# Optimization experiments

Hardware: AMD Instinct MI355X
Metric: run time of the kernel (lower is better)

The kernel has to match this reference:

```python
import jax, jax.numpy as jnp
import numpy as np

D_DIM, H_DIM, W_DIM = 8, 16, 16
HIDDEN, HEAD = 256, 32
NUM_HEADS = HIDDEN // HEAD


def _rel_indices(D, H, W):
    # 3D relative coordinate indices into the bias table, shape (N, N) each.
    coords = np.stack(np.meshgrid(np.arange(D), np.arange(H), np.arange(W), indexing='ij'),
                      axis=-1).reshape(-1, 3)
    rel = coords[:, None, :] - coords[None, :, :]
    rel[:, :, 0] += D - 1
    rel[:, :, 1] += H - 1
    rel[:, :, 2] += W - 1
    return jnp.asarray(rel[:, :, 0]), jnp.asarray(rel[:, :, 1]), jnp.asarray(rel[:, :, 2])


def setup_inputs() -> dict:
    key = jax.random.key(0)
    ks = jax.random.split(key, 6)
    B = 4
    x = jax.random.normal(ks[0], (B, D_DIM, H_DIM, W_DIM, HIDDEN), dtype=jnp.float32)
    s = 1.0 / np.sqrt(HIDDEN)
    Wq = jax.random.normal(ks[1], (HIDDEN, HIDDEN), dtype=jnp.float32) * s
    Wk = jax.random.normal(ks[2], (HIDDEN, HIDDEN), dtype=jnp.float32) * s
    Wv = jax.random.normal(ks[3], (HIDDEN, HIDDEN), dtype=jnp.float32) * s
    Wo = jax.random.normal(ks[4], (HIDDEN, HIDDEN), dtype=jnp.float32) * s
    bias_table = jax.random.normal(ks[5], (NUM_HEADS, 2 * D_DIM - 1, 2 * H_DIM - 1, 2 * W_DIM - 1),
                                   dtype=jnp.float32) * 0.02
    return {"x": x, "Wq": Wq, "Wk": Wk, "Wv": Wv, "Wo": Wo, "bias_table": bias_table}


def reference(x, Wq, Wk, Wv, Wo, bias_table):
    B, D, H, W, C = x.shape
    N = D * H * W
    rd, rh, rw = _rel_indices(D, H, W)
    # gathered relative-position bias: (num_heads, N, N)
    bias = bias_table[:, rd, rh, rw]

    xf = x.reshape(B, N, C)
    q = (xf @ Wq).reshape(B, N, NUM_HEADS, HEAD).transpose(0, 2, 1, 3)  # b h n d
    k = (xf @ Wk).reshape(B, N, NUM_HEADS, HEAD).transpose(0, 2, 1, 3)
    v = (xf @ Wv).reshape(B, N, NUM_HEADS, HEAD).transpose(0, 2, 1, 3)

    scores = jnp.einsum('bhnd,bhmd->bhnm', q, k) / jnp.sqrt(jnp.float32(HEAD))
    scores = scores + bias[None]  # broadcast over batch
    attn = jax.nn.softmax(scores, axis=-1)
    out = jnp.einsum('bhnm,bhmd->bhnd', attn, v)
    out = out.transpose(0, 2, 1, 3).reshape(B, N, HIDDEN) @ Wo
    return out.reshape(B, D, H, W, HIDDEN)
```

## Files before the change

kernel.cpp:

```cpp
#include <hip/hip_runtime.h>
#include <math.h>

#define HIDDEN 256
#define NHEADS 8
#define HEAD 32
#define NTOK 2048
#define NBIAS 115320
#define HTAB 14415

typedef __attribute__((ext_vector_type(8))) __bf16 bf16x8;
typedef __attribute__((ext_vector_type(4))) float f32x4;
typedef __attribute__((ext_vector_type(16))) float f32x16;
typedef __attribute__((ext_vector_type(4))) unsigned uint32x4;

static __device__ __forceinline__ f32x4 mfma16(bf16x8 a, bf16x8 b, f32x4 c) {
    return __builtin_amdgcn_mfma_f32_16x16x32_bf16(a, b, c, 0, 0, 0);
}
static __device__ __forceinline__ f32x16 mfma32(bf16x8 a, bf16x8 b, f32x16 c) {
    return __builtin_amdgcn_mfma_f32_32x32x16_bf16(a, b, c, 0, 0, 0);
}
static __device__ __forceinline__ float fexp2(float x) {
#if __has_builtin(__builtin_amdgcn_exp2f)
    return __builtin_amdgcn_exp2f(x);
#else
    return exp2f(x);
#endif
}
static __device__ __forceinline__ unsigned pkbf16(float a, float b) {
    unsigned short ua = __builtin_bit_cast(unsigned short, (__bf16)a);
    unsigned short ub = __builtin_bit_cast(unsigned short, (__bf16)b);
    return (unsigned)ua | ((unsigned)ub << 16);
}

__global__ void k_cvt_x(const float* __restrict__ x, __bf16* __restrict__ xb) {
    int i = (blockIdx.x * blockDim.x + threadIdx.x) * 4;
    float4 v = *(const float4*)(x + i);
    xb[i + 0] = (__bf16)v.x;
    xb[i + 1] = (__bf16)v.y;
    xb[i + 2] = (__bf16)v.z;
    xb[i + 3] = (__bf16)v.w;
}

__global__ void k_cvt_w(const float* __restrict__ w0, const float* __restrict__ w1,
                        const float* __restrict__ w2, const float* __restrict__ w3,
                        __bf16* __restrict__ t0, __bf16* __restrict__ t1,
                        __bf16* __restrict__ t2, __bf16* __restrict__ t3) {
    int wsel = blockIdx.x >> 8;
    int i = (blockIdx.x & 255) * 256 + threadIdx.x;
    const float* w = (wsel == 0) ? w0 : (wsel == 1) ? w1 : (wsel == 2) ? w2 : w3;
    __bf16* t = (wsel == 0) ? t0 : (wsel == 1) ? t1 : (wsel == 2) ? t2 : t3;
    int n = i >> 8, k = i & 255;
    t[i] = (__bf16)w[k * 256 + n];
}

__global__ __launch_bounds__(256) void k_qkv(const __bf16* __restrict__ xb,
                                             const __bf16* __restrict__ wqT,
                                             const __bf16* __restrict__ wkT,
                                             const __bf16* __restrict__ wvT,
                                             __bf16* __restrict__ qb,
                                             __bf16* __restrict__ kb,
                                             __bf16* __restrict__ vb) {
    int wid = blockIdx.x * 4 + (threadIdx.x >> 6);
    int lane = threadIdx.x & 63;
    int ng = wid % 12, mt = wid / 12;
    int lm = lane & 15, lg = lane >> 4, lk = lg * 8;
    int which = ng >> 2;
    int nc0 = (ng & 3) * 64;
    const __bf16* wT = (which == 0) ? wqT : (which == 1) ? wkT : wvT;

    f32x4 acc[4][4];
#pragma unroll
    for (int m = 0; m < 4; ++m)
#pragma unroll
        for (int n = 0; n < 4; ++n) acc[m][n] = (f32x4){0.f, 0.f, 0.f, 0.f};

    const __bf16* arow = xb + (size_t)(mt * 64 + lm) * 256 + lk;
    const __bf16* brow = wT + (size_t)(nc0 + lm) * 256 + lk;
#pragma unroll
    for (int kk = 0; kk < 8; ++kk) {
        bf16x8 a[4], b[4];
#pragma unroll
        for (int m = 0; m < 4; ++m) a[m] = *(const bf16x8*)(arow + (size_t)m * 16 * 256 + kk * 32);
#pragma unroll
        for (int n = 0; n < 4; ++n) b[n] = *(const bf16x8*)(brow + (size_t)n * 16 * 256 + kk * 32);
#pragma unroll
        for (int m = 0; m < 4; ++m)
#pragma unroll
            for (int n = 0; n < 4; ++n) acc[m][n] = mfma16(a[m], b[n], acc[m][n]);
    }
    const float QS = 0.17677669529663687f * 1.4426950408889634f;
#pragma unroll
    for (int m = 0; m < 4; ++m) {
#pragma unroll
        for (int n = 0; n < 4; ++n) {
            int col = nc0 + n * 16 + lm;
            int h = col >> 5, d = col & 31;
#pragma unroll
            for (int r = 0; r < 4; ++r) {
                int row = mt * 64 + m * 16 + lg * 4 + r;
                int b_ = row >> 11, tr = row & 2047;
                size_t bh = (size_t)(b_ * 8 + h) * 65536;
                if (which == 0) {
                    qb[bh + (size_t)tr * 32 + d] = (__bf16)(acc[m][n][r] * QS);
                } else if (which == 1) {
                    size_t idx = ((size_t)(tr >> 5) * 128 + (d >> 4) * 64 + ((d >> 3) & 1) * 32 + (tr & 31)) * 8 + (d & 7);
                    kb[bh + idx] = (__bf16)acc[m][n][r];
                } else {
                    size_t idx = ((size_t)(tr >> 5) * 256 + ((tr >> 3) & 3) * 64 + ((tr >> 2) & 1) * 32 + d) * 4 + (tr & 3);
                    vb[bh + idx] = (__bf16)acc[m][n][r];
                }
            }
        }
    }
}

__global__ __launch_bounds__(256) void k_attn(const __bf16* __restrict__ qb,
                                              const __bf16* __restrict__ kb,
                                              const __bf16* __restrict__ vb,
                                              const float* __restrict__ bias,
                                              __bf16* __restrict__ attn) {
    int i = blockIdx.x;
    int bh = (i & 7) + ((i >> 9) << 3);
    int qs = (i >> 3) & 63;
    int b_ = bh >> 3, h = bh & 7;
    int w = threadIdx.x >> 6;
    int lane = threadIdx.x & 63;
    int lq = lane & 31;
    int hf = lane >> 5;
    int q0 = qs * 32;

    __shared__ float smem[4488];

    {
        int qd = q0 >> 8, qh0 = (q0 >> 4) & 15;
        const float* bt = bias + h * HTAB;
        for (int t = threadIdx.x; t < 4488; t += 256) {
            int dd = t / 561, rem = t - dd * 561;
            int hh = rem / 33, ww = rem - hh * 33;
            int dw = 30 - ww; if (dw < 0) dw = 0;
            smem[t] = bt[(qd + dd) * 961 + (qh0 + hh) * 31 + dw] * 1.4426950408889634f;
        }
    }
    __syncthreads();

    const __bf16* qbase = qb + (size_t)bh * NTOK * 32;
    const __bf16* kbase = kb + (size_t)bh * NTOK * 32;
    const __bf16* vbase = vb + (size_t)bh * NTOK * 32;

    bf16x8 qf0 = *(const bf16x8*)(qbase + (size_t)(q0 + lq) * 32 + hf * 8);
    bf16x8 qf1 = *(const bf16x8*)(qbase + (size_t)(q0 + lq) * 32 + 16 + hf * 8);

    int lbase = (lq >> 4) * 33 + 15 - (lq & 15) + 4 * hf;

    f32x16 Oacc, Lacc;
#pragma unroll
    for (int j = 0; j < 16; ++j) { Oacc[j] = 0.f; Lacc[j] = 0.f; }

    bf16x8 ones;
#pragma unroll
    for (int j = 0; j < 8; ++j) ones[j] = (__bf16)1.0f;

    bf16x8 ck0, ck1;
    {
        const __bf16* kt = kbase + ((size_t)(w * 16) * 128 + lane) * 8;
        ck0 = *(const bf16x8*)(kt);
        ck1 = *(const bf16x8*)(kt + 512);
    }

#pragma unroll
    for (int it = 0; it < 16; ++it) {
        int t0 = w * 512 + it * 32;
        int tt = t0 >> 5;

        bf16x8 nk0, nk1;
        if (it < 15) {
            const __bf16* kt1 = kbase + ((size_t)(tt + 1) * 128 + lane) * 8;
            nk0 = *(const bf16x8*)(kt1);
            nk1 = *(const bf16x8*)(kt1 + 512);
        }

        const __bf16* vt = vbase + ((size_t)tt * 256 + lane) * 4;
        uint2 va  = *(const uint2*)(vt);
        uint2 vbq = *(const uint2*)(vt + 256);
        uint2 vc  = *(const uint2*)(vt + 512);
        uint2 vd  = *(const uint2*)(vt + 768);
        uint32x4 vw0 = {va.x, va.y, vbq.x, vbq.y};
        uint32x4 vw1 = {vc.x, vc.y, vd.x, vd.y};
        bf16x8 vf0 = __builtin_bit_cast(bf16x8, vw0);
        bf16x8 vf1 = __builtin_bit_cast(bf16x8, vw1);

        int kd = t0 >> 8, kh0 = (t0 >> 4) & 15;
        int a0 = (7 - kd) * 561 + (15 - kh0) * 33 + lbase;
        f32x16 S;
#pragma unroll
        for (int r = 0; r < 4; ++r) {
            S[r]      = smem[a0 + r];
            S[4 + r]  = smem[a0 + 8 + r];
            S[8 + r]  = smem[a0 - 33 + r];
            S[12 + r] = smem[a0 - 25 + r];
        }
        S = mfma32(ck0, qf0, S);
        S = mfma32(ck1, qf1, S);

        unsigned W0 = pkbf16(fexp2(S[0]),  fexp2(S[1]));
        unsigned W1 = pkbf16(fexp2(S[2]),  fexp2(S[3]));
        unsigned W2 = pkbf16(fexp2(S[4]),  fexp2(S[5]));
        unsigned W3 = pkbf16(fexp2(S[6]),  fexp2(S[7]));
        unsigned W4 = pkbf16(fexp2(S[8]),  fexp2(S[9]));
        unsigned W5 = pkbf16(fexp2(S[10]), fexp2(S[11]));
        unsigned W6 = pkbf16(fexp2(S[12]), fexp2(S[13]));
        unsigned W7 = pkbf16(fexp2(S[14]), fexp2(S[15]));
        uint32x4 pw0 = {W0, W1, W2, W3};
        uint32x4 pw1 = {W4, W5, W6, W7};
        bf16x8 pf0 = __builtin_bit_cast(bf16x8, pw0);
        bf16x8 pf1 = __builtin_bit_cast(bf16x8, pw1);

        Oacc = mfma32(vf0, pf0, Oacc);
        Oacc = mfma32(vf1, pf1, Oacc);
        Lacc = mfma32(ones, pf0, Lacc);
        Lacc = mfma32(ones, pf1, Lacc);

        if (it < 15) { ck0 = nk0; ck1 = nk1; }
    }

    __syncthreads();
    float (*part)[64][17] = (float (*)[64][17])smem;
#pragma unroll
    for (int j = 0; j < 4; ++j) {
        float4 t;
        t.x = Oacc[4 * j]; t.y = Oacc[4 * j + 1]; t.z = Oacc[4 * j + 2]; t.w = Oacc[4 * j + 3];
        *(float4*)&part[w][lane][4 * j] = t;
    }
    part[w][lane][16] = Lacc[0];
    __syncthreads();

    float4 o = {0.f, 0.f, 0.f, 0.f};
    float ls = 0.f;
#pragma unroll
    for (int sw = 0; sw < 4; ++sw) {
        float4 t = *(const float4*)&part[sw][lane][4 * w];
        o.x += t.x; o.y += t.y; o.z += t.z; o.w += t.w;
        ls += part[sw][lane][16];
    }
    float inv = 1.0f / ls;
    unsigned lo = pkbf16(o.x * inv, o.y * inv);
    unsigned hi = pkbf16(o.z * inv, o.w * inv);
    size_t base = ((size_t)b_ * NTOK + q0 + lq) * 256 + h * 32 + 8 * w + 4 * hf;
    *(uint2*)(attn + base) = make_uint2(lo, hi);
}

__global__ __launch_bounds__(256) void k_out(const __bf16* __restrict__ attn,
                                             const __bf16* __restrict__ woT,
                                             float* __restrict__ out) {
    int wid = blockIdx.x * 4 + (threadIdx.x >> 6);
    int lane = threadIdx.x & 63;
    int ng = wid & 3, mt = wid >> 2;
    int lm = lane & 15, lg = lane >> 4, lk = lg * 8;
    int nc0 = ng * 64;

    f32x4 acc[4][4];
#pragma unroll
    for (int m = 0; m < 4; ++m)
#pragma unroll
        for (int n = 0; n < 4; ++n) acc[m][n] = (f32x4){0.f, 0.f, 0.f, 0.f};

    const __bf16* arow = attn + (size_t)(mt * 64 + lm) * 256 + lk;
    const __bf16* brow = woT + (size_t)(nc0 + lm) * 256 + lk;
#pragma unroll
    for (int kk = 0; kk < 8; ++kk) {
        bf16x8 a[4], b[4];
#pragma unroll
        for (int m = 0; m < 4; ++m) a[m] = *(const bf16x8*)(arow + (size_t)m * 16 * 256 + kk * 32);
#pragma unroll
        for (int n = 0; n < 4; ++n) b[n] = *(const bf16x8*)(brow + (size_t)n * 16 * 256 + kk * 32);
#pragma unroll
        for (int m = 0; m < 4; ++m)
#pragma unroll
            for (int n = 0; n < 4; ++n) acc[m][n] = mfma16(a[m], b[n], acc[m][n]);
    }
#pragma unroll
    for (int m = 0; m < 4; ++m) {
#pragma unroll
        for (int n = 0; n < 4; ++n) {
            int col = nc0 + n * 16 + lm;
#pragma unroll
            for (int r = 0; r < 4; ++r) {
                int row = mt * 64 + m * 16 + lg * 4 + r;
                out[(size_t)row * 256 + col] = acc[m][n][r];
            }
        }
    }
}

extern "C" void kernel_launch(void* const* d_in, const int* in_sizes, int n_in,
                              void* d_out, int out_size, void* d_ws, size_t ws_size,
                              hipStream_t stream) {
    const float* x    = (const float*)d_in[0];
    const float* Wq   = (const float*)d_in[1];
    const float* Wk   = (const float*)d_in[2];
    const float* Wv   = (const float*)d_in[3];
    const float* Wo   = (const float*)d_in[4];
    const float* bias = (const float*)d_in[5];
    float* out = (float*)d_out;

    __bf16* ws  = (__bf16*)d_ws;
    __bf16* xb  = ws;
    __bf16* wqT = xb  + 2097152;
    __bf16* wkT = wqT + 65536;
    __bf16* wvT = wkT + 65536;
    __bf16* woT = wvT + 65536;
    __bf16* qb  = woT + 65536;
    __bf16* kb  = qb  + 2097152;
    __bf16* vb  = kb  + 2097152;
    __bf16* att = xb;

    k_cvt_x<<<2048, 256, 0, stream>>>(x, xb);
    k_cvt_w<<<1024, 256, 0, stream>>>(Wq, Wk, Wv, Wo, wqT, wkT, wvT, woT);
    k_qkv<<<384, 256, 0, stream>>>(xb, wqT, wkT, wvT, qb, kb, vb);
    k_attn<<<2048, 256, 0, stream>>>(qb, kb, vb, bias, att);
    k_out<<<128, 256, 0, stream>>>(att, woT, out);
}
```

Measured before the change: 86.95 us.

## Process two 32-query tiles per attention block to reuse K/V loads

Each attention block now handles 64 queries as two 32-row tiles sharing the same K and V fragments per iteration, halving the grid to 1024 blocks. The bias slice in shared memory grows to cover the extra query rows, and the cross-wave reduction runs twice. This is meant to halve global K/V traffic per query and give more independent MFMA work per wave, at the cost of more registers (four accumulators), less parallelism, and an extra barrier round.

```diff
diff --git a/kernel.cpp b/kernel.cpp
--- a/kernel.cpp
+++ b/kernel.cpp
@@ -120,22 +120,23 @@
                                               const float* __restrict__ bias,
                                               __bf16* __restrict__ attn) {
     int i = blockIdx.x;
-    int bh = (i & 7) + ((i >> 9) << 3);
-    int qs = (i >> 3) & 63;
+    int x = i & 7, r_ = i >> 3;
+    int bh = x + ((r_ >> 5) << 3);
+    int qblk = r_ & 31;
     int b_ = bh >> 3, h = bh & 7;
     int w = threadIdx.x >> 6;
     int lane = threadIdx.x & 63;
     int lq = lane & 31;
     int hf = lane >> 5;
-    int q0 = qs * 32;
-
-    __shared__ float smem[4488];
+    int q0 = qblk * 64;
+
+    __shared__ float smem[5016];
 
     {
         int qd = q0 >> 8, qh0 = (q0 >> 4) & 15;
         const float* bt = bias + h * HTAB;
-        for (int t = threadIdx.x; t < 4488; t += 256) {
-            int dd = t / 561, rem = t - dd * 561;
+        for (int t = threadIdx.x; t < 5016; t += 256) {
+            int dd = t / 627, rem = t - dd * 627;
             int hh = rem / 33, ww = rem - hh * 33;
             int dw = 30 - ww; if (dw < 0) dw = 0;
             smem[t] = bt[(qd + dd) * 961 + (qh0 + hh) * 31 + dw] * 1.4426950408889634f;
@@ -147,14 +148,16 @@
     const __bf16* kbase = kb + (size_t)bh * NTOK * 32;
     const __bf16* vbase = vb + (size_t)bh * NTOK * 32;
 
-    bf16x8 qf0 = *(const bf16x8*)(qbase + (size_t)(q0 + lq) * 32 + hf * 8);
-    bf16x8 qf1 = *(const bf16x8*)(qbase + (size_t)(q0 + lq) * 32 + 16 + hf * 8);
+    bf16x8 qfA0 = *(const bf16x8*)(qbase + (size_t)(q0 + lq) * 32 + hf * 8);
+    bf16x8 qfA1 = *(const bf16x8*)(qbase + (size_t)(q0 + lq) * 32 + 16 + hf * 8);
+    bf16x8 qfB0 = *(const bf16x8*)(qbase + (size_t)(q0 + 32 + lq) * 32 + hf * 8);
+    bf16x8 qfB1 = *(const bf16x8*)(qbase + (size_t)(q0 + 32 + lq) * 32 + 16 + hf * 8);
 
     int lbase = (lq >> 4) * 33 + 15 - (lq & 15) + 4 * hf;
 
-    f32x16 Oacc, Lacc;
-#pragma unroll
-    for (int j = 0; j < 16; ++j) { Oacc[j] = 0.f; Lacc[j] = 0.f; }
+    f32x16 OaccA, LaccA, OaccB, LaccB;
+#pragma unroll
+    for (int j = 0; j < 16; ++j) { OaccA[j] = 0.f; LaccA[j] = 0.f; OaccB[j] = 0.f; LaccB[j] = 0.f; }
 
     bf16x8 ones;
 #pragma unroll
@@ -190,63 +193,93 @@
         bf16x8 vf1 = __builtin_bit_cast(bf16x8, vw1);
 
         int kd = t0 >> 8, kh0 = (t0 >> 4) & 15;
-        int a0 = (7 - kd) * 561 + (15 - kh0) * 33 + lbase;
-        f32x16 S;
+        int a0 = (7 - kd) * 627 + (15 - kh0) * 33 + lbase;
+        f32x16 SA, SB;
 #pragma unroll
         for (int r = 0; r < 4; ++r) {
-            S[r]      = smem[a0 + r];
-            S[4 + r]  = smem[a0 + 8 + r];
-            S[8 + r]  = smem[a0 - 33 + r];
-            S[12 + r] = smem[a0 - 25 + r];
-        }
-        S = mfma32(ck0, qf0, S);
-        S = mfma32(ck1, qf1, S);
-
-        unsigned W0 = pkbf16(fexp2(S[0]),  fexp2(S[1]));
-        unsigned W1 = pkbf16(fexp2(S[2]),  fexp2(S[3]));
-        unsigned W2 = pkbf16(fexp2(S[4]),  fexp2(S[5]));
-        unsigned W3 = pkbf16(fexp2(S[6]),  fexp2(S[7]));
-        unsigned W4 = pkbf16(fexp2(S[8]),  fexp2(S[9]));
-        unsigned W5 = pkbf16(fexp2(S[10]), fexp2(S[11]));
-        unsigned W6 = pkbf16(fexp2(S[12]), fexp2(S[13]));
-        unsigned W7 = pkbf16(fexp2(S[14]), fexp2(S[15]));
-        uint32x4 pw0 = {W0, W1, W2, W3};
-        uint32x4 pw1 = {W4, W5, W6, W7};
-        bf16x8 pf0 = __builtin_bit_cast(bf16x8, pw0);
-        bf16x8 pf1 = __builtin_bit_cast(bf16x8, pw1);
-
-        Oacc = mfma32(vf0, pf0, Oacc);
-        Oacc = mfma32(vf1, pf1, Oacc);
-        Lacc = mfma32(ones, pf0, Lacc);
-        Lacc = mfma32(ones, pf1, Lacc);
+            SA[r]      = smem[a0 + r];
+            SA[4 + r]  = smem[a0 + 8 + r];
+            SA[8 + r]  = smem[a0 - 33 + r];
+            SA[12 + r] = smem[a0 - 25 + r];
+            SB[r]      = smem[a0 + 66 + r];
+            SB[4 + r]  = smem[a0 + 74 + r];
+            SB[8 + r]  = smem[a0 + 33 + r];
+            SB[12 + r] = smem[a0 + 41 + r];
+        }
+        SA = mfma32(ck0, qfA0, SA);
+        SA = mfma32(ck1, qfA1, SA);
+        SB = mfma32(ck0, qfB0, SB);
+        SB = mfma32(ck1, qfB1, SB);
+
+        {
+            unsigned W0 = pkbf16(fexp2(SA[0]),  fexp2(SA[1]));
+            unsigned W1 = pkbf16(fexp2(SA[2]),  fexp2(SA[3]));
+            unsigned W2 = pkbf16(fexp2(SA[4]),  fexp2(SA[5]));
+            unsigned W3 = pkbf16(fexp2(SA[6]),  fexp2(SA[7]));
+            unsigned W4 = pkbf16(fexp2(SA[8]),  fexp2(SA[9]));
+            unsigned W5 = pkbf16(fexp2(SA[10]), fexp2(SA[11]));
+            unsigned W6 = pkbf16(fexp2(SA[12]), fexp2(SA[13]));
+            unsigned W7 = pkbf16(fexp2(SA[14]), fexp2(SA[15]));
+            uint32x4 pw0 = {W0, W1, W2, W3};
+            uint32x4 pw1 = {W4, W5, W6, W7};
+            bf16x8 pf0 = __builtin_bit_cast(bf16x8, pw0);
+            bf16x8 pf1 = __builtin_bit_cast(bf16x8, pw1);
+            OaccA = mfma32(vf0, pf0, OaccA);
+            OaccA = mfma32(vf1, pf1, OaccA);
+            LaccA = mfma32(ones, pf0, LaccA);
+            LaccA = mfma32(ones, pf1, LaccA);
+        }
+        {
+            unsigned W0 = pkbf16(fexp2(SB[0]),  fexp2(SB[1]));
+            unsigned W1 = pkbf16(fexp2(SB[2]),  fexp2(SB[3]));
+            unsigned W2 = pkbf16(fexp2(SB[4]),  fexp2(SB[5]));
+            unsigned W3 = pkbf16(fexp2(SB[6]),  fexp2(SB[7]));
+            unsigned W4 = pkbf16(fexp2(SB[8]),  fexp2(SB[9]));
+            unsigned W5 = pkbf16(fexp2(SB[10]), fexp2(SB[11]));
+            unsigned W6 = pkbf16(fexp2(SB[12]), fexp2(SB[13]));
+            unsigned W7 = pkbf16(fexp2(SB[14]), fexp2(SB[15]));
+            uint32x4 pw0 = {W0, W1, W2, W3};
+            uint32x4 pw1 = {W4, W5, W6, W7};
+            bf16x8 pf0 = __builtin_bit_cast(bf16x8, pw0);
+            bf16x8 pf1 = __builtin_bit_cast(bf16x8, pw1);
+            OaccB = mfma32(vf0, pf0, OaccB);
+            OaccB = mfma32(vf1, pf1, OaccB);
+            LaccB = mfma32(ones, pf0, LaccB);
+            LaccB = mfma32(ones, pf1, LaccB);
+        }
 
         if (it < 15) { ck0 = nk0; ck1 = nk1; }
     }
 
-    __syncthreads();
     float (*part)[64][17] = (float (*)[64][17])smem;
 #pragma unroll
-    for (int j = 0; j < 4; ++j) {
-        float4 t;
-        t.x = Oacc[4 * j]; t.y = Oacc[4 * j + 1]; t.z = Oacc[4 * j + 2]; t.w = Oacc[4 * j + 3];
-        *(float4*)&part[w][lane][4 * j] = t;
-    }
-    part[w][lane][16] = Lacc[0];
-    __syncthreads();
-
-    float4 o = {0.f, 0.f, 0.f, 0.f};
-    float ls = 0.f;
-#pragma unroll
-    for (int sw = 0; sw < 4; ++sw) {
-        float4 t = *(const float4*)&part[sw][lane][4 * w];
-        o.x += t.x; o.y += t.y; o.z += t.z; o.w += t.w;
-        ls += part[sw][lane][16];
-    }
-    float inv = 1.0f / ls;
-    unsigned lo = pkbf16(o.x * inv, o.y * inv);
-    unsigned hi = pkbf16(o.z * inv, o.w * inv);
-    size_t base = ((size_t)b_ * NTOK + q0 + lq) * 256 + h * 32 + 8 * w + 4 * hf;
-    *(uint2*)(attn + base) = make_uint2(lo, hi);
+    for (int s = 0; s < 2; ++s) {
+        f32x16* O = s ? &OaccB : &OaccA;
+        f32x16* L = s ? &LaccB : &LaccA;
+        __syncthreads();
+#pragma unroll
+        for (int j = 0; j < 4; ++j) {
+            float4 t;
+            t.x = (*O)[4 * j]; t.y = (*O)[4 * j + 1]; t.z = (*O)[4 * j + 2]; t.w = (*O)[4 * j + 3];
+            *(float4*)&part[w][lane][4 * j] = t;
+        }
+        part[w][lane][16] = (*L)[0];
+        __syncthreads();
+
+        float4 o = {0.f, 0.f, 0.f, 0.f};
+        float ls = 0.f;
+#pragma unroll
+        for (int sw = 0; sw < 4; ++sw) {
+            float4 t = *(const float4*)&part[sw][lane][4 * w];
+            o.x += t.x; o.y += t.y; o.z += t.z; o.w += t.w;
+            ls += part[sw][lane][16];
+        }
+        float inv = 1.0f / ls;
+        unsigned lo = pkbf16(o.x * inv, o.y * inv);
+        unsigned hi = pkbf16(o.z * inv, o.w * inv);
+        size_t base = ((size_t)b_ * NTOK + q0 + 32 * s + lq) * 256 + h * 32 + 8 * w + 4 * hf;
+        *(uint2*)(attn + base) = make_uint2(lo, hi);
+    }
 }
 
 __global__ __launch_bounds__(256) void k_out(const __bf16* __restrict__ attn,
@@ -317,6 +350,6 @@
     k_cvt_x<<<2048, 256, 0, stream>>>(x, xb);
     k_cvt_w<<<1024, 256, 0, stream>>>(Wq, Wk, Wv, Wo, wqT, wkT, wvT, woT);
     k_qkv<<<384, 256, 0, stream>>>(xb, wqT, wkT, wvT, qb, kb, vb);
-    k_attn<<<2048, 256, 0, stream>>>(qb, kb, vb, bias, att);
+    k_attn<<<1024, 256, 0, stream>>>(qb, kb, vb, bias, att);
     k_out<<<128, 256, 0, stream>>>(att, woT, out);
 }
```

Result: faster. 84.17 us (-3.2%).
